# Optimization experiments

Measured on AMD Instinct MI355X. Metric: run time of the kernel, lower is better.

The kernel has to match this reference:

```python
import jax, jax.numpy as jnp
import numpy as np

INPUT_SIZE = 1024
HIDDEN_SIZE = 512
MEM_BANK = 100
N_IMG = 32768


def setup_inputs() -> dict:
    key = jax.random.key(0)
    ks = jax.random.split(key, 16)
    I, H, M = INPUT_SIZE, HIDDEN_SIZE, MEM_BANK
    D = I + H  # concat([x_t, h_t]) feature dim
    s = 0.01   # matches init_weights normal_(0.0, 0.01); Linears use similar small init
    return {
        "hidden_frames": jax.random.normal(ks[0], (N_IMG, I), dtype=jnp.float32),
        # hidden_to_content: Linear(D, H)
        "Wc": jax.random.normal(ks[1], (D, H), dtype=jnp.float32) * s,
        "bc": jnp.zeros((H,), dtype=jnp.float32),
        # write_gate: Linear(D, 1)
        "Wwg": jax.random.normal(ks[2], (D, 1), dtype=jnp.float32) * s,
        "bwg": jnp.zeros((1,), dtype=jnp.float32),
        # write_prob: Linear(D, M)
        "Wwp": jax.random.normal(ks[3], (D, M), dtype=jnp.float32) * s,
        "bwp": jnp.zeros((M,), dtype=jnp.float32),
        # read_gate: Linear(D, 1)
        "Wrg": jax.random.normal(ks[4], (D, 1), dtype=jnp.float32) * s,
        "brg": jnp.zeros((1,), dtype=jnp.float32),
        # read_prob: Linear(D, M)
        "Wrp": jax.random.normal(ks[5], (D, M), dtype=jnp.float32) * s,
        "brp": jnp.zeros((M,), dtype=jnp.float32),
        # recurrent params
        "Wxh": jax.random.normal(ks[6], (I, H), dtype=jnp.float32) * s,
        "Wrh": jax.random.normal(ks[7], (H, H), dtype=jnp.float32) * s,
        "Whh": jax.random.normal(ks[8], (H, H), dtype=jnp.float32) * s,
        "bh": jnp.zeros((H,), dtype=jnp.float32),
        "nImg": N_IMG,
    }


def _run(hidden_frames, Wc, bc, Wwg, bwg, Wwp, bwp, Wrg, brg, Wrp, brp, Wxh, Wrh, Whh, bh, nImg):
    M, H = Wwp.shape[1], Wxh.shape[1]
    mem0 = jnp.zeros((M, H), dtype=hidden_frames.dtype)
    h0 = jnp.zeros((H,), dtype=hidden_frames.dtype)

    def step(carry, x_t):
        mem, h = carry                                   # mem: [M,H], h: [H]
        xh = jnp.concatenate([x_t, h])                   # [I+H]
        ar = jax.nn.softmax(xh @ Wrp + brp)              # read address [M]
        go = jax.nn.sigmoid(xh @ Wrg + brg)              # read gate [1]
        r = go * (ar @ mem)                              # gated read [H]
        h_new = jax.nn.relu(x_t @ Wxh + r @ Wrh + h @ Whh + bh)
        c = jax.nn.relu(xh @ Wc + bc)                    # write content [H]
        aw = jax.nn.softmax(xh @ Wwp + bwp)              # write address [M]
        gw = jax.nn.sigmoid(xh @ Wwg + bwg)              # write gate [1]
        mem_new = gw * aw[:, None] * c[None, :] + (1.0 - aw[:, None]) * mem
        return (mem_new, h_new), h_new

    xs = hidden_frames[:nImg]
    _, hiddens = jax.lax.scan(step, (mem0, h0), xs)      # [nImg, H]
    return hiddens


def reference(hidden_frames, Wc, bc, Wwg, bwg, Wwp, bwp, Wrg, brg, Wrp, brp, Wxh, Wrh, Whh, bh, nImg):
    return _run(hidden_frames, Wc, bc, Wwg, bwg, Wwp, bwp, Wrg, brg, Wrp, brp, Wxh, Wrh, Whh, bh, nImg)
```

## Files before the change

### kernel.cpp

```cpp
#include <hip/hip_runtime.h>
#include <hip/hip_bf16.h>

#define NWG 32
#define TSEQ 512
#define JW 16
#define HH 512
#define II 1024
#define GSTRIDE 1280
#define CHK 48

#define OFF_REC    4096u
#define OFF_WSTACK (1u<<20)
#define OFF_G      (16u<<20)

typedef float fx4 __attribute__((ext_vector_type(4)));

__device__ __forceinline__ float bf2f(__hip_bfloat16 x){ return __bfloat162float(x); }
__device__ __forceinline__ unsigned f2u(float x){ return __builtin_bit_cast(unsigned, x); }
__device__ __forceinline__ float u2f(unsigned x){ return __builtin_bit_cast(float, x); }

__device__ __forceinline__ void ld_chunk3(const fx4* p0, const fx4* p1, const fx4* p2,
                                          fx4& a, fx4& b, fx4& c){
  asm volatile("global_load_dwordx4 %0, %3, off sc1\n\t"
               "global_load_dwordx4 %1, %4, off sc1\n\t"
               "global_load_dwordx4 %2, %5, off sc1\n\t"
               "s_waitcnt vmcnt(0)"
               : "=&v"(a), "=&v"(b), "=&v"(c)
               : "v"(p0), "v"(p1), "v"(p2) : "memory");
}
__device__ __forceinline__ void st_chunk(fx4* p, fx4 v){
  asm volatile("global_store_dwordx4 %0, %1, off sc1" :: "v"(p), "v"(v) : "memory");
}

__device__ __forceinline__ float red32(float v){
  v += __shfl_xor(v, 16); v += __shfl_xor(v, 8); v += __shfl_xor(v, 4);
  v += __shfl_xor(v, 2);  v += __shfl_xor(v, 1);
  return v;
}
__device__ __forceinline__ float redsum64(float v){
  v += __shfl_xor(v, 32); v += __shfl_xor(v, 16); v += __shfl_xor(v, 8);
  v += __shfl_xor(v, 4);  v += __shfl_xor(v, 2);  v += __shfl_xor(v, 1);
  return v;
}
__device__ __forceinline__ float redmax64(float v){
  v = fmaxf(v, __shfl_xor(v, 32)); v = fmaxf(v, __shfl_xor(v, 16));
  v = fmaxf(v, __shfl_xor(v, 8));  v = fmaxf(v, __shfl_xor(v, 4));
  v = fmaxf(v, __shfl_xor(v, 2));  v = fmaxf(v, __shfl_xor(v, 1));
  return v;
}

__global__ void pack_kernel(const float* __restrict__ Wxh, const float* __restrict__ bh,
                            const float* __restrict__ Wc,  const float* __restrict__ bc,
                            const float* __restrict__ Wrp, const float* __restrict__ brp,
                            const float* __restrict__ Wwp, const float* __restrict__ bwp,
                            const float* __restrict__ Wrg, const float* __restrict__ brg,
                            const float* __restrict__ Wwg, const float* __restrict__ bwg,
                            float* __restrict__ Wstack)
{
  int n = blockIdx.x*256 + threadIdx.x;
  int k = blockIdx.y;
  if (n >= GSTRIDE) return;
  float v = 0.f;
  if (k < II) {
    if (n < 512)       v = Wxh[k*512 + n];
    else if (n < 1024) v = Wc[k*512 + (n-512)];
    else if (n < 1124) v = Wrp[k*100 + (n-1024)];
    else if (n < 1224) v = Wwp[k*100 + (n-1124)];
    else if (n == 1224) v = Wrg[k];
    else if (n == 1225) v = Wwg[k];
  } else {
    if (n < 512)       v = bh[n];
    else if (n < 1024) v = bc[n-512];
    else if (n < 1124) v = brp[n-1024];
    else if (n < 1224) v = bwp[n-1124];
    else if (n == 1224) v = brg[0];
    else if (n == 1225) v = bwg[0];
  }
  Wstack[k*GSTRIDE + n] = v;
}

__global__ __launch_bounds__(256) void gemm_kernel(const float* __restrict__ X,
                                                   const float* __restrict__ Wstack,
                                                   __hip_bfloat16* __restrict__ G)
{
  __shared__ float As[16][68];
  __shared__ float Bs[16][64];
  const int tid = threadIdx.x;
  const int row0 = blockIdx.y*64, col0 = blockIdx.x*64;
  const int ty = tid>>4, tx = tid&15;
  const int amm = tid>>2, akk = (tid&3)<<2;
  const int bkk = tid>>4, bnn = (tid&15)<<2;
  float acc[4][4] = {{0.f}};
  for (int k0 = 0; k0 < II; k0 += 16) {
    float4 av = *(const float4*)(X + (size_t)(row0+amm)*II + k0 + akk);
    float4 bv = *(const float4*)(Wstack + (size_t)(k0+bkk)*GSTRIDE + col0 + bnn);
    __syncthreads();
    As[akk+0][amm]=av.x; As[akk+1][amm]=av.y; As[akk+2][amm]=av.z; As[akk+3][amm]=av.w;
    *(float4*)&Bs[bkk][bnn] = bv;
    __syncthreads();
#pragma unroll
    for (int kk=0; kk<16; kk++){
      float4 a = *(float4*)&As[kk][ty<<2];
      float4 b = *(float4*)&Bs[kk][tx<<2];
      acc[0][0] += a.x*b.x; acc[0][1] += a.x*b.y; acc[0][2] += a.x*b.z; acc[0][3] += a.x*b.w;
      acc[1][0] += a.y*b.x; acc[1][1] += a.y*b.y; acc[1][2] += a.y*b.z; acc[1][3] += a.y*b.w;
      acc[2][0] += a.z*b.x; acc[2][1] += a.z*b.y; acc[2][2] += a.z*b.z; acc[2][3] += a.z*b.w;
      acc[3][0] += a.w*b.x; acc[3][1] += a.w*b.y; acc[3][2] += a.w*b.z; acc[3][3] += a.w*b.w;
    }
  }
#pragma unroll
  for (int i2=0;i2<4;i2++){
    int r = row0 + (ty<<2) + i2;
#pragma unroll
    for (int j2=0;j2<4;j2++){
      int cidx = col0 + (tx<<2) + j2;
      float v = acc[i2][j2] + Wstack[(size_t)II*GSTRIDE + cidx];
      G[(size_t)r*GSTRIDE + cidx] = __float2bfloat16(v);
    }
  }
}

__global__ __launch_bounds__(TSEQ) void seq_kernel(
    const float* __restrict__ Wc,  const float* __restrict__ Wwg,
    const float* __restrict__ Wwp, const float* __restrict__ Wrg,
    const float* __restrict__ Wrp, const float* __restrict__ Wrh,
    const float* __restrict__ Whh,
    const __hip_bfloat16* __restrict__ G,
    float* __restrict__ out,
    fx4* rec4, int N)
{
  const int w = blockIdx.x;
  const int t = threadIdx.x;
  const int j = t >> 5;
  const int l = t & 31;
  const int jg = w*JW + j;

  __shared__ fx4 raw4[NWG*CHK];
  __shared__ float pubbuf[144];
  __shared__ float ht[JW];
  __shared__ float e_ar[104], aw_n[104];
  __shared__ float part6[4][104];
  __shared__ float part2[4][128];
  __shared__ float memW[JW][104];
  __shared__ float Wrp_sl[JW][104];
  __shared__ float Wwp_sl[4][HH];
  __shared__ float scal_s[2];

  const float* rawf = (const float*)raw4;

  float whh_r[16], wch_r[16], wrh_r[16];
#pragma unroll
  for (int i=0;i<16;i++){
    int k = i*32 + l;
    whh_r[i] = Whh[(size_t)k*HH + jg];
    wch_r[i] = Wc[(size_t)(II+k)*HH + jg];
    wrh_r[i] = Wrh[(size_t)k*HH + jg];
  }
  for (int idx=t; idx<JW*104; idx+=TSEQ){
    int kl = idx/104, m = idx - kl*104;
    int kgl = II + w*JW + kl;
    float v = 0.f;
    if (m < 100) v = Wrp[(size_t)kgl*100 + m];
    else if (m == 100) v = Wrg[kgl];
    Wrp_sl[kl][m] = v;
    memW[kl][m] = 0.f;
  }
  for (int idx=t; idx<4*HH; idx+=TSEQ){
    int ci = idx>>9, k = idx&511;
    int cg = ci*32 + w;
    float v = 0.f;
    if (cg < 100) v = Wwp[(size_t)(II+k)*100 + cg];
    else if (cg == 100) v = Wwg[II+k];
    Wwp_sl[ci][k] = v;
  }
  if (t < 144) pubbuf[t] = 0.f;
  __syncthreads();

  if (t < JW) {
    float hv = fmaxf(0.f, bf2f(G[(size_t)0*GSTRIDE + w*JW + t]));
    float cv = fmaxf(0.f, bf2f(G[(size_t)0*GSTRIDE + 512 + w*JW + t]));
    ht[t] = hv;
    pubbuf[t] = hv;
    pubbuf[16+t] = cv;
    out[(size_t)0*HH + w*JW + t] = hv;
  }
  __syncthreads();
  if (t < 101) {
    float s = 0.f;
#pragma unroll
    for (int kl=0; kl<16; kl++) s += ht[kl]*Wrp_sl[kl][t];
    pubbuf[32+t] = s;
  }
  __syncthreads();
  if (t < CHK) {
    fx4 v;
    v.x = pubbuf[3*t]; v.y = pubbuf[3*t+1]; v.z = pubbuf[3*t+2];
    v.w = u2f(1u);
    st_chunk(rec4 + (size_t)w*CHK + t, v);
  }

  for (int step=1; step<N; ++step) {
    const unsigned tg = (unsigned)step;
    float g_rp0=0.f, g_rp1=0.f, g_aw0=0.f, g_aw1=0.f, g_h=0.f, g_c=0.f;
    {
      const __hip_bfloat16* Grow = G + (size_t)step*GSTRIDE;
      if (t < 64) {
        g_rp0 = bf2f(Grow[1024+t]);
        int m2 = t+64;
        g_rp1 = bf2f(Grow[m2==100 ? 1224 : 1024+m2]);
      } else if (t < 128) {
        const __hip_bfloat16* Gpr = G + (size_t)(step-1)*GSTRIDE;
        int u = t-64;
        g_aw0 = bf2f(Gpr[1124+u]);
        int m2 = u+64;
        g_aw1 = bf2f(Gpr[m2==100 ? 1225 : 1124+m2]);
      }
      if (l == 0) { g_h = bf2f(Grow[jg]); g_c = bf2f(Grow[512+jg]); }
    }
    {
      const fx4* prev4 = rec4 + (size_t)((step&1)^1)*NWG*CHK;
      const fx4 *p0 = prev4 + t, *p1 = prev4 + t + 512, *p2 = prev4 + t + 1024;
      fx4 a, b, c;
      ld_chunk3(p0, p1, p2, a, b, c);
      while (f2u(a.w) != tg || f2u(b.w) != tg || f2u(c.w) != tg)
        ld_chunk3(p0, p1, p2, a, b, c);
      raw4[t] = a; raw4[t+512] = b; raw4[t+1024] = c;
    }
    __syncthreads();
    if (t < 404) {
      int m = t % 101, q = t / 101;
      int off = ((32+m)/3)*4 + (32+m)%3;
      const float* base = rawf + (size_t)q*8*192 + off;
      float s = ((base[0*192]+base[1*192])+(base[2*192]+base[3*192]))
              + ((base[4*192]+base[5*192])+(base[6*192]+base[7*192]));
      part6[q][m] = s;
    }
    float ph=0.f, pc=0.f, pw=0.f;
    {
      int l15 = l & 15, lh = l >> 4;
      int coh = (l15/3)*4 + l15%3;
      int coc = ((16+l15)/3)*4 + (16+l15)%3;
      const float* mh = rawf + lh*192;
#pragma unroll
      for (int i=0;i<16;i++){
        float hv = mh[384*i + coh];
        float cv2 = mh[384*i + coc];
        ph += whh_r[i]*hv;
        pc += wch_r[i]*hv;
        pw += wrh_r[i]*cv2;
      }
      ph = red32(ph); pc = red32(pc); pw = red32(pw);
    }
    {
      int ci = t >> 7, li = t & 127;
      float s = 0.f;
#pragma unroll
      for (int ii=0; ii<4; ii++){
        int k = li + 128*ii;
        float hv = rawf[(k>>4)*192 + ((k&15)/3)*4 + (k&15)%3];
        s += hv * Wwp_sl[ci][k];
      }
      part2[ci][li] = s;
    }
    __syncthreads();
    if (t < 64) {
      int u = t, m2 = u+64;
      float v0 = part6[0][u]+part6[1][u]+part6[2][u]+part6[3][u] + g_rp0;
      float v1 = (m2 <= 100) ? (part6[0][m2]+part6[1][m2]+part6[2][m2]+part6[3][m2] + g_rp1)
                             : -1e30f;
      float vs1 = (m2 < 100) ? v1 : -1e30f;
      float mx = redmax64(fmaxf(v0, vs1));
      float e0 = __expf(v0 - mx), e1 = __expf(vs1 - mx);
      e_ar[u] = e0;
      if (m2 < 104) e_ar[m2] = e1;
      float ssum = redsum64(e0 + e1);
      float r100 = __shfl(v1, 36);
      if (u == 0) scal_s[0] = (1.f/(1.f+__expf(-r100))) / ssum;
    } else if (t < 128) {
      int u = t-64, m2 = u+64;
      int wi0 = u&31, ci0 = u>>5, p0i = 133+ci0;
      float v0 = rawf[wi0*192 + (p0i/3)*4 + p0i%3] + g_aw0;
      float v1 = -1e30f;
      if (m2 <= 100) {
        int wi1 = m2&31, ci1 = m2>>5, p1i = 133+ci1;
        v1 = rawf[wi1*192 + (p1i/3)*4 + p1i%3] + g_aw1;
      }
      float vs1 = (m2 < 100) ? v1 : -1e30f;
      float mx = redmax64(fmaxf(v0, vs1));
      float e0 = __expf(v0 - mx), e1 = __expf(vs1 - mx);
      float ssum = redsum64(e0 + e1);
      aw_n[u] = e0 / ssum;
      if (m2 < 104) aw_n[m2] = e1 / ssum;
      float r100 = __shfl(v1, 36);
      if (u == 0) scal_s[1] = 1.f/(1.f+__expf(-r100));
    } else if (t < 384) {
      int wv = t >> 6;
      int ci = wv - 2, ln = t & 63;
      float s = part2[ci][ln] + part2[ci][ln+64];
      s = redsum64(s);
      if (ln == 0 && (ci*32 + w) < 101) pubbuf[133+ci] = s;
    }
    __syncthreads();
    {
      float gws = scal_s[1], gos = scal_s[0];
      float rwp = 0.f;
#pragma unroll
      for (int q=0; q<4; q++){
        int m = l + 32*q;
        if (m < 100) {
          float a2 = aw_n[m];
          float mv = memW[j][m];
          mv = (1.f - a2)*mv + gws*a2*pw;
          memW[j][m] = mv;
          rwp += e_ar[m]*mv;
        }
      }
      rwp = red32(rwp);
      float hv = fmaxf(0.f, g_h + ph + gos*rwp);
      if (l == 0) {
        float cv = fmaxf(0.f, g_c + pc);
        ht[j] = hv;
        pubbuf[j] = hv;
        pubbuf[16+j] = cv;
        out[(size_t)step*HH + jg] = hv;
      }
    }
    if (step + 1 < N) {
      __syncthreads();
      if (t < 101) {
        float s = 0.f;
#pragma unroll
        for (int kl=0; kl<16; kl++) s += ht[kl]*Wrp_sl[kl][t];
        pubbuf[32+t] = s;
      }
      __syncthreads();
      if (t < CHK) {
        fx4 v;
        v.x = pubbuf[3*t]; v.y = pubbuf[3*t+1]; v.z = pubbuf[3*t+2];
        v.w = u2f((unsigned)(step+1));
        st_chunk(rec4 + (size_t)((step&1)*NWG + w)*CHK + t, v);
      }
    }
  }
}

extern "C" void kernel_launch(void* const* d_in, const int* in_sizes, int n_in,
                              void* d_out, int out_size, void* d_ws, size_t ws_size,
                              hipStream_t stream) {
  const float* X   = (const float*)d_in[0];
  const float* Wc  = (const float*)d_in[1];
  const float* bc  = (const float*)d_in[2];
  const float* Wwg = (const float*)d_in[3];
  const float* bwg = (const float*)d_in[4];
  const float* Wwp = (const float*)d_in[5];
  const float* bwp = (const float*)d_in[6];
  const float* Wrg = (const float*)d_in[7];
  const float* brg = (const float*)d_in[8];
  const float* Wrp = (const float*)d_in[9];
  const float* brp = (const float*)d_in[10];
  const float* Wxh = (const float*)d_in[11];
  const float* Wrh = (const float*)d_in[12];
  const float* Whh = (const float*)d_in[13];
  const float* bh  = (const float*)d_in[14];

  const int N = in_sizes[0] / II;

  char* ws = (char*)d_ws;
  fx4* rec4 = (fx4*)(ws + OFF_REC);
  float* Wstack = (float*)(ws + OFF_WSTACK);
  __hip_bfloat16* G = (__hip_bfloat16*)(ws + OFF_G);
  float* out = (float*)d_out;

  pack_kernel<<<dim3(GSTRIDE/256, II+1), 256, 0, stream>>>(
      Wxh, bh, Wc, bc, Wrp, brp, Wwp, bwp, Wrg, brg, Wwg, bwg, Wstack);

  gemm_kernel<<<dim3(GSTRIDE/64, N/64), 256, 0, stream>>>(X, Wstack, G);

  seq_kernel<<<NWG, TSEQ, 0, stream>>>(
      Wc, Wwg, Wwp, Wrg, Wrp, Wrh, Whh, G, out,
      rec4, N);
}
```

Before: 118.6 ms.

## Shrink published recurrent state and compute read-address dot product redundantly per workgroup

Each workgroup now publishes only its h, c and write-prob partials (12 chunks instead of 48) rather than its partial h·Wrp sums. Each workgroup instead recomputes the full h·Wrp read-address logits itself, using 128 Wrp weights held in registers per thread. This cuts the global polling traffic and removes one block barrier per step from the serial critical path. In exchange it adds redundant compute and raises register pressure, which may cause spills.

```diff
diff --git a/kernel.cpp b/kernel.cpp
--- a/kernel.cpp
+++ b/kernel.cpp
@@ -7,7 +7,7 @@
 #define HH 512
 #define II 1024
 #define GSTRIDE 1280
-#define CHK 48
+#define CHK 12
 
 #define OFF_REC    4096u
 #define OFF_WSTACK (1u<<20)
@@ -19,14 +19,10 @@
 __device__ __forceinline__ unsigned f2u(float x){ return __builtin_bit_cast(unsigned, x); }
 __device__ __forceinline__ float u2f(unsigned x){ return __builtin_bit_cast(float, x); }
 
-__device__ __forceinline__ void ld_chunk3(const fx4* p0, const fx4* p1, const fx4* p2,
-                                          fx4& a, fx4& b, fx4& c){
-  asm volatile("global_load_dwordx4 %0, %3, off sc1\n\t"
-               "global_load_dwordx4 %1, %4, off sc1\n\t"
-               "global_load_dwordx4 %2, %5, off sc1\n\t"
+__device__ __forceinline__ void ld_chunk1(const fx4* p, fx4& a){
+  asm volatile("global_load_dwordx4 %0, %1, off sc1\n\t"
                "s_waitcnt vmcnt(0)"
-               : "=&v"(a), "=&v"(b), "=&v"(c)
-               : "v"(p0), "v"(p1), "v"(p2) : "memory");
+               : "=&v"(a) : "v"(p) : "memory");
 }
 __device__ __forceinline__ void st_chunk(fx4* p, fx4 v){
   asm volatile("global_store_dwordx4 %0, %1, off sc1" :: "v"(p), "v"(v) : "memory");
@@ -135,18 +131,14 @@
   const int l = t & 31;
   const int jg = w*JW + j;
 
-  __shared__ fx4 raw4[NWG*CHK];
-  __shared__ float pubbuf[144];
-  __shared__ float ht[JW];
+  __shared__ __align__(16) float rec_f[NWG][40];
+  __shared__ float pubbuf[36];
   __shared__ float e_ar[104], aw_n[104];
-  __shared__ float part6[4][104];
+  __shared__ float part_ar[4][104];
   __shared__ float part2[4][128];
   __shared__ float memW[JW][104];
-  __shared__ float Wrp_sl[JW][104];
   __shared__ float Wwp_sl[4][HH];
   __shared__ float scal_s[2];
-
-  const float* rawf = (const float*)raw4;
 
   float whh_r[16], wch_r[16], wrh_r[16];
 #pragma unroll
@@ -156,13 +148,18 @@
     wch_r[i] = Wc[(size_t)(II+k)*HH + jg];
     wrh_r[i] = Wrh[(size_t)k*HH + jg];
   }
+  const int mq_m = t % 101;
+  const int mq_q = t / 101;
+  float wrp_r[128];
+  if (t < 404) {
+#pragma unroll
+    for (int i=0;i<128;i++){
+      int kg = II + mq_q*128 + i;
+      wrp_r[i] = (mq_m < 100) ? Wrp[(size_t)kg*100 + mq_m] : Wrg[kg];
+    }
+  }
   for (int idx=t; idx<JW*104; idx+=TSEQ){
     int kl = idx/104, m = idx - kl*104;
-    int kgl = II + w*JW + kl;
-    float v = 0.f;
-    if (m < 100) v = Wrp[(size_t)kgl*100 + m];
-    else if (m == 100) v = Wrg[kgl];
-    Wrp_sl[kl][m] = v;
     memW[kl][m] = 0.f;
   }
   for (int idx=t; idx<4*HH; idx+=TSEQ){
@@ -173,23 +170,15 @@
     else if (cg == 100) v = Wwg[II+k];
     Wwp_sl[ci][k] = v;
   }
-  if (t < 144) pubbuf[t] = 0.f;
+  if (t < 36) pubbuf[t] = 0.f;
   __syncthreads();
 
   if (t < JW) {
     float hv = fmaxf(0.f, bf2f(G[(size_t)0*GSTRIDE + w*JW + t]));
     float cv = fmaxf(0.f, bf2f(G[(size_t)0*GSTRIDE + 512 + w*JW + t]));
-    ht[t] = hv;
     pubbuf[t] = hv;
     pubbuf[16+t] = cv;
     out[(size_t)0*HH + w*JW + t] = hv;
-  }
-  __syncthreads();
-  if (t < 101) {
-    float s = 0.f;
-#pragma unroll
-    for (int kl=0; kl<16; kl++) s += ht[kl]*Wrp_sl[kl][t];
-    pubbuf[32+t] = s;
   }
   __syncthreads();
   if (t < CHK) {
@@ -217,34 +206,39 @@
       }
       if (l == 0) { g_h = bf2f(Grow[jg]); g_c = bf2f(Grow[512+jg]); }
     }
-    {
-      const fx4* prev4 = rec4 + (size_t)((step&1)^1)*NWG*CHK;
-      const fx4 *p0 = prev4 + t, *p1 = prev4 + t + 512, *p2 = prev4 + t + 1024;
-      fx4 a, b, c;
-      ld_chunk3(p0, p1, p2, a, b, c);
-      while (f2u(a.w) != tg || f2u(b.w) != tg || f2u(c.w) != tg)
-        ld_chunk3(p0, p1, p2, a, b, c);
-      raw4[t] = a; raw4[t+512] = b; raw4[t+1024] = c;
+    if (t < NWG*CHK) {
+      const fx4* p = rec4 + (size_t)((step&1)^1)*NWG*CHK + t;
+      fx4 a;
+      ld_chunk1(p, a);
+      while (f2u(a.w) != tg) ld_chunk1(p, a);
+      int wgsrc = t / CHK, ci = t - wgsrc*CHK;
+      float* dst = &rec_f[wgsrc][3*ci];
+      dst[0] = a.x; dst[1] = a.y; dst[2] = a.z;
     }
     __syncthreads();
     if (t < 404) {
-      int m = t % 101, q = t / 101;
-      int off = ((32+m)/3)*4 + (32+m)%3;
-      const float* base = rawf + (size_t)q*8*192 + off;
-      float s = ((base[0*192]+base[1*192])+(base[2*192]+base[3*192]))
-              + ((base[4*192]+base[5*192])+(base[6*192]+base[7*192]));
-      part6[q][m] = s;
+      float s0=0.f, s1=0.f, s2=0.f, s3=0.f;
+#pragma unroll
+      for (int bw=0; bw<8; bw++){
+        const fx4* hp = (const fx4*)&rec_f[mq_q*8 + bw][0];
+#pragma unroll
+        for (int ii=0; ii<4; ii++){
+          fx4 h4 = hp[ii];
+          s0 += h4.x*wrp_r[bw*16 + ii*4 + 0];
+          s1 += h4.y*wrp_r[bw*16 + ii*4 + 1];
+          s2 += h4.z*wrp_r[bw*16 + ii*4 + 2];
+          s3 += h4.w*wrp_r[bw*16 + ii*4 + 3];
+        }
+      }
+      part_ar[mq_q][mq_m] = (s0+s1)+(s2+s3);
     }
     float ph=0.f, pc=0.f, pw=0.f;
     {
-      int l15 = l & 15, lh = l >> 4;
-      int coh = (l15/3)*4 + l15%3;
-      int coc = ((16+l15)/3)*4 + (16+l15)%3;
-      const float* mh = rawf + lh*192;
 #pragma unroll
       for (int i=0;i<16;i++){
-        float hv = mh[384*i + coh];
-        float cv2 = mh[384*i + coc];
+        int k = i*32 + l;
+        float hv  = rec_f[k>>4][k&15];
+        float cv2 = rec_f[k>>4][16+(k&15)];
         ph += whh_r[i]*hv;
         pc += wch_r[i]*hv;
         pw += wrh_r[i]*cv2;
@@ -257,16 +251,15 @@
 #pragma unroll
       for (int ii=0; ii<4; ii++){
         int k = li + 128*ii;
-        float hv = rawf[(k>>4)*192 + ((k&15)/3)*4 + (k&15)%3];
-        s += hv * Wwp_sl[ci][k];
+        s += rec_f[k>>4][k&15] * Wwp_sl[ci][k];
       }
       part2[ci][li] = s;
     }
     __syncthreads();
     if (t < 64) {
       int u = t, m2 = u+64;
-      float v0 = part6[0][u]+part6[1][u]+part6[2][u]+part6[3][u] + g_rp0;
-      float v1 = (m2 <= 100) ? (part6[0][m2]+part6[1][m2]+part6[2][m2]+part6[3][m2] + g_rp1)
+      float v0 = part_ar[0][u]+part_ar[1][u]+part_ar[2][u]+part_ar[3][u] + g_rp0;
+      float v1 = (m2 <= 100) ? (part_ar[0][m2]+part_ar[1][m2]+part_ar[2][m2]+part_ar[3][m2] + g_rp1)
                              : -1e30f;
       float vs1 = (m2 < 100) ? v1 : -1e30f;
       float mx = redmax64(fmaxf(v0, vs1));
@@ -278,13 +271,9 @@
       if (u == 0) scal_s[0] = (1.f/(1.f+__expf(-r100))) / ssum;
     } else if (t < 128) {
       int u = t-64, m2 = u+64;
-      int wi0 = u&31, ci0 = u>>5, p0i = 133+ci0;
-      float v0 = rawf[wi0*192 + (p0i/3)*4 + p0i%3] + g_aw0;
+      float v0 = rec_f[u&31][32+(u>>5)] + g_aw0;
       float v1 = -1e30f;
-      if (m2 <= 100) {
-        int wi1 = m2&31, ci1 = m2>>5, p1i = 133+ci1;
-        v1 = rawf[wi1*192 + (p1i/3)*4 + p1i%3] + g_aw1;
-      }
+      if (m2 <= 100) v1 = rec_f[m2&31][32+(m2>>5)] + g_aw1;
       float vs1 = (m2 < 100) ? v1 : -1e30f;
       float mx = redmax64(fmaxf(v0, vs1));
       float e0 = __expf(v0 - mx), e1 = __expf(vs1 - mx);
@@ -298,7 +287,7 @@
       int ci = wv - 2, ln = t & 63;
       float s = part2[ci][ln] + part2[ci][ln+64];
       s = redsum64(s);
-      if (ln == 0 && (ci*32 + w) < 101) pubbuf[133+ci] = s;
+      if (ln == 0 && (ci*32 + w) < 101) pubbuf[32+ci] = s;
     }
     __syncthreads();
     {
@@ -319,20 +308,12 @@
       float hv = fmaxf(0.f, g_h + ph + gos*rwp);
       if (l == 0) {
         float cv = fmaxf(0.f, g_c + pc);
-        ht[j] = hv;
         pubbuf[j] = hv;
         pubbuf[16+j] = cv;
         out[(size_t)step*HH + jg] = hv;
       }
     }
     if (step + 1 < N) {
-      __syncthreads();
-      if (t < 101) {
-        float s = 0.f;
-#pragma unroll
-        for (int kl=0; kl<16; kl++) s += ht[kl]*Wrp_sl[kl][t];
-        pubbuf[32+t] = s;
-      }
       __syncthreads();
       if (t < CHK) {
         fx4 v;
```

New measurement: 138.5 ms. 16.8% more time.

## Split cross-workgroup record into critical h/c part and deferred read-projection part

Applied to the files above, without the earlier changes.

Each workgroup's published record is split into a small 12-chunk part (h, c, write-prob partials) and a 34-chunk part (read-prob partials). The critical part is stored before the Wrp projection and is polled first. The larger part is loaded asynchronously while the h/c matvecs and write-prob partials run, which hides part of the inter-workgroup latency. It also drops the strided index arithmetic by using plain 2D LDS layouts. The cost is an extra barrier and a second spin-wait on the larger chunk set.

```diff
diff --git a/kernel.cpp b/kernel.cpp
--- a/kernel.cpp
+++ b/kernel.cpp
@@ -7,7 +7,9 @@
 #define HH 512
 #define II 1024
 #define GSTRIDE 1280
-#define CHK 48
+#define REC 48
+#define CHK1 12
+#define CHK2 34
 
 #define OFF_REC    4096u
 #define OFF_WSTACK (1u<<20)
@@ -19,14 +21,16 @@
 __device__ __forceinline__ unsigned f2u(float x){ return __builtin_bit_cast(unsigned, x); }
 __device__ __forceinline__ float u2f(unsigned x){ return __builtin_bit_cast(float, x); }
 
-__device__ __forceinline__ void ld_chunk3(const fx4* p0, const fx4* p1, const fx4* p2,
-                                          fx4& a, fx4& b, fx4& c){
-  asm volatile("global_load_dwordx4 %0, %3, off sc1\n\t"
-               "global_load_dwordx4 %1, %4, off sc1\n\t"
-               "global_load_dwordx4 %2, %5, off sc1\n\t"
+__device__ __forceinline__ void ld_chunk1(const fx4* p, fx4& a){
+  asm volatile("global_load_dwordx4 %0, %1, off sc1\n\t"
                "s_waitcnt vmcnt(0)"
-               : "=&v"(a), "=&v"(b), "=&v"(c)
-               : "v"(p0), "v"(p1), "v"(p2) : "memory");
+               : "=&v"(a) : "v"(p) : "memory");
+}
+__device__ __forceinline__ void ld_chunk_async(const fx4* p, fx4& a){
+  asm volatile("global_load_dwordx4 %0, %1, off sc1" : "=&v"(a) : "v"(p) : "memory");
+}
+__device__ __forceinline__ void wait_vm3(fx4& a, fx4& b, fx4& c){
+  asm volatile("s_waitcnt vmcnt(0)" : "+v"(a), "+v"(b), "+v"(c) :: "memory");
 }
 __device__ __forceinline__ void st_chunk(fx4* p, fx4 v){
   asm volatile("global_store_dwordx4 %0, %1, off sc1" :: "v"(p), "v"(v) : "memory");
@@ -135,8 +139,10 @@
   const int l = t & 31;
   const int jg = w*JW + j;
 
-  __shared__ fx4 raw4[NWG*CHK];
-  __shared__ float pubbuf[144];
+  __shared__ __align__(16) float raw1[NWG][40];
+  __shared__ float raw2[NWG][104];
+  __shared__ float pubbuf[36];
+  __shared__ float pub2[104];
   __shared__ float ht[JW];
   __shared__ float e_ar[104], aw_n[104];
   __shared__ float part6[4][104];
@@ -146,8 +152,6 @@
   __shared__ float Wwp_sl[4][HH];
   __shared__ float scal_s[2];
 
-  const float* rawf = (const float*)raw4;
-
   float whh_r[16], wch_r[16], wrh_r[16];
 #pragma unroll
   for (int i=0;i<16;i++){
@@ -173,7 +177,8 @@
     else if (cg == 100) v = Wwg[II+k];
     Wwp_sl[ci][k] = v;
   }
-  if (t < 144) pubbuf[t] = 0.f;
+  if (t < 36) pubbuf[t] = 0.f;
+  if (t < 104) pub2[t] = 0.f;
   __syncthreads();
 
   if (t < JW) {
@@ -189,15 +194,26 @@
     float s = 0.f;
 #pragma unroll
     for (int kl=0; kl<16; kl++) s += ht[kl]*Wrp_sl[kl][t];
-    pubbuf[32+t] = s;
+    pub2[t] = s;
   }
   __syncthreads();
-  if (t < CHK) {
-    fx4 v;
-    v.x = pubbuf[3*t]; v.y = pubbuf[3*t+1]; v.z = pubbuf[3*t+2];
+  if (t < CHK1) {
+    fx4 v; v.x = pubbuf[3*t]; v.y = pubbuf[3*t+1]; v.z = pubbuf[3*t+2];
     v.w = u2f(1u);
-    st_chunk(rec4 + (size_t)w*CHK + t, v);
-  }
+    st_chunk(rec4 + (size_t)w*REC + t, v);
+  }
+  if (t < CHK2) {
+    fx4 v; v.x = pub2[3*t]; v.y = pub2[3*t+1]; v.z = pub2[3*t+2];
+    v.w = u2f(1u);
+    st_chunk(rec4 + (size_t)w*REC + CHK1 + t, v);
+  }
+
+  const int wA = t/CHK2,        cjA = t - wA*CHK2;
+  const int wB = (t+512)/CHK2,  cjB = (t+512) - wB*CHK2;
+  const int wC = (t+1024)/CHK2, cjC = (t+1024) - wC*CHK2;
+  const int offA = wA*REC + CHK1 + cjA;
+  const int offB = wB*REC + CHK1 + cjB;
+  const int offC = wC*REC + CHK1 + cjC;
 
   for (int step=1; step<N; ++step) {
     const unsigned tg = (unsigned)step;
@@ -217,34 +233,29 @@
       }
       if (l == 0) { g_h = bf2f(Grow[jg]); g_c = bf2f(Grow[512+jg]); }
     }
-    {
-      const fx4* prev4 = rec4 + (size_t)((step&1)^1)*NWG*CHK;
-      const fx4 *p0 = prev4 + t, *p1 = prev4 + t + 512, *p2 = prev4 + t + 1024;
-      fx4 a, b, c;
-      ld_chunk3(p0, p1, p2, a, b, c);
-      while (f2u(a.w) != tg || f2u(b.w) != tg || f2u(c.w) != tg)
-        ld_chunk3(p0, p1, p2, a, b, c);
-      raw4[t] = a; raw4[t+512] = b; raw4[t+1024] = c;
-    }
-    __syncthreads();
-    if (t < 404) {
-      int m = t % 101, q = t / 101;
-      int off = ((32+m)/3)*4 + (32+m)%3;
-      const float* base = rawf + (size_t)q*8*192 + off;
-      float s = ((base[0*192]+base[1*192])+(base[2*192]+base[3*192]))
-              + ((base[4*192]+base[5*192])+(base[6*192]+base[7*192]));
-      part6[q][m] = s;
-    }
+    const fx4* prev4 = rec4 + (size_t)((step&1)^1)*NWG*REC;
+    if (t < NWG*CHK1) {
+      int sw = t / CHK1, ci = t - sw*CHK1;
+      const fx4* p = prev4 + sw*REC + ci;
+      fx4 a;
+      ld_chunk1(p, a);
+      while (f2u(a.w) != tg) ld_chunk1(p, a);
+      float* dst = &raw1[sw][3*ci];
+      dst[0] = a.x; dst[1] = a.y; dst[2] = a.z;
+    }
+    __syncthreads();
+    fx4 a0, a1, a2 = {0.f,0.f,0.f,0.f};
+    const fx4 *pA = prev4 + offA, *pB = prev4 + offB, *pC = prev4 + offC;
+    ld_chunk_async(pA, a0);
+    ld_chunk_async(pB, a1);
+    if (t < 64) ld_chunk_async(pC, a2);
     float ph=0.f, pc=0.f, pw=0.f;
     {
-      int l15 = l & 15, lh = l >> 4;
-      int coh = (l15/3)*4 + l15%3;
-      int coc = ((16+l15)/3)*4 + (16+l15)%3;
-      const float* mh = rawf + lh*192;
 #pragma unroll
       for (int i=0;i<16;i++){
-        float hv = mh[384*i + coh];
-        float cv2 = mh[384*i + coc];
+        int k = i*32 + l;
+        float hv  = raw1[k>>4][k&15];
+        float cv2 = raw1[k>>4][16+(k&15)];
         ph += whh_r[i]*hv;
         pc += wch_r[i]*hv;
         pw += wrh_r[i]*cv2;
@@ -257,10 +268,25 @@
 #pragma unroll
       for (int ii=0; ii<4; ii++){
         int k = li + 128*ii;
-        float hv = rawf[(k>>4)*192 + ((k&15)/3)*4 + (k&15)%3];
-        s += hv * Wwp_sl[ci][k];
+        s += raw1[k>>4][k&15] * Wwp_sl[ci][k];
       }
       part2[ci][li] = s;
+    }
+    {
+      wait_vm3(a0, a1, a2);
+      while (f2u(a0.w) != tg) ld_chunk1(pA, a0);
+      while (f2u(a1.w) != tg) ld_chunk1(pB, a1);
+      if (t < 64) { while (f2u(a2.w) != tg) ld_chunk1(pC, a2); }
+      float* d0 = &raw2[wA][3*cjA]; d0[0]=a0.x; d0[1]=a0.y; d0[2]=a0.z;
+      float* d1 = &raw2[wB][3*cjB]; d1[0]=a1.x; d1[1]=a1.y; d1[2]=a1.z;
+      if (t < 64) { float* d2 = &raw2[wC][3*cjC]; d2[0]=a2.x; d2[1]=a2.y; d2[2]=a2.z; }
+    }
+    __syncthreads();
+    if (t < 404) {
+      int m = t % 101, q = t / 101;
+      const float* b = &raw2[q*8][0] + m;
+      float s = ((b[0]+b[104])+(b[208]+b[312])) + ((b[416]+b[520])+(b[624]+b[728]));
+      part6[q][m] = s;
     }
     __syncthreads();
     if (t < 64) {
@@ -278,13 +304,9 @@
       if (u == 0) scal_s[0] = (1.f/(1.f+__expf(-r100))) / ssum;
     } else if (t < 128) {
       int u = t-64, m2 = u+64;
-      int wi0 = u&31, ci0 = u>>5, p0i = 133+ci0;
-      float v0 = rawf[wi0*192 + (p0i/3)*4 + p0i%3] + g_aw0;
+      float v0 = raw1[u&31][32+(u>>5)] + g_aw0;
       float v1 = -1e30f;
-      if (m2 <= 100) {
-        int wi1 = m2&31, ci1 = m2>>5, p1i = 133+ci1;
-        v1 = rawf[wi1*192 + (p1i/3)*4 + p1i%3] + g_aw1;
-      }
+      if (m2 <= 100) v1 = raw1[m2&31][32+(m2>>5)] + g_aw1;
       float vs1 = (m2 < 100) ? v1 : -1e30f;
       float mx = redmax64(fmaxf(v0, vs1));
       float e0 = __expf(v0 - mx), e1 = __expf(vs1 - mx);
@@ -298,7 +320,7 @@
       int ci = wv - 2, ln = t & 63;
       float s = part2[ci][ln] + part2[ci][ln+64];
       s = redsum64(s);
-      if (ln == 0 && (ci*32 + w) < 101) pubbuf[133+ci] = s;
+      if (ln == 0 && (ci*32 + w) < 101) pubbuf[32+ci] = s;
     }
     __syncthreads();
     {
@@ -327,18 +349,23 @@
     }
     if (step + 1 < N) {
       __syncthreads();
+      fx4* cur4 = rec4 + (size_t)((step&1)*NWG + w)*REC;
+      if (t < CHK1) {
+        fx4 v; v.x = pubbuf[3*t]; v.y = pubbuf[3*t+1]; v.z = pubbuf[3*t+2];
+        v.w = u2f((unsigned)(step+1));
+        st_chunk(cur4 + t, v);
+      }
       if (t < 101) {
         float s = 0.f;
 #pragma unroll
         for (int kl=0; kl<16; kl++) s += ht[kl]*Wrp_sl[kl][t];
-        pubbuf[32+t] = s;
+        pub2[t] = s;
       }
       __syncthreads();
-      if (t < CHK) {
-        fx4 v;
-        v.x = pubbuf[3*t]; v.y = pubbuf[3*t+1]; v.z = pubbuf[3*t+2];
+      if (t < CHK2) {
+        fx4 v; v.x = pub2[3*t]; v.y = pub2[3*t+1]; v.z = pub2[3*t+2];
         v.w = u2f((unsigned)(step+1));
-        st_chunk(rec4 + (size_t)((step&1)*NWG + w)*CHK + t, v);
+        st_chunk(cur4 + CHK1 + t, v);
       }
     }
   }
```

Measured after the change: 113.6 ms. -4.2%, faster.
